# Kernel tuning notes

Measured on AMD Instinct MI355X. Metric: run time of the kernel, lower is better.

The kernel has to match this reference:

```python
import jax, jax.numpy as jnp
import numpy as np

B, T, I, H = 512, 512, 128, 256
EPS = 1e-5


def setup_inputs() -> dict:
    key = jax.random.key(0)
    ks = jax.random.split(key, 8)
    s_ih = 1.0 / np.sqrt(H)
    padded_X = jax.random.normal(ks[0], (B, T, I), dtype=jnp.float32)
    lengths = jax.random.randint(ks[1], (B,), 1, T + 1)  # in [1, T]
    # PyTorch LSTM params: W_ih (4H, I), W_hh (4H, H), biases (4H,), gate order [i,f,g,o]
    W_ih = jax.random.uniform(ks[2], (4 * H, I), minval=-s_ih, maxval=s_ih, dtype=jnp.float32)
    W_hh = jax.random.uniform(ks[3], (4 * H, H), minval=-s_ih, maxval=s_ih, dtype=jnp.float32)
    b_ih = jax.random.uniform(ks[4], (4 * H,), minval=-s_ih, maxval=s_ih, dtype=jnp.float32)
    b_hh = jax.random.uniform(ks[5], (4 * H,), minval=-s_ih, maxval=s_ih, dtype=jnp.float32)
    gamma = jnp.ones((H,), dtype=jnp.float32)
    beta = jnp.zeros((H,), dtype=jnp.float32)
    return {"padded_X": padded_X, "lengths": lengths, "W_ih": W_ih, "W_hh": W_hh,
            "b_ih": b_ih, "b_hh": b_hh, "gamma": gamma, "beta": beta}


def _lstm_last_hidden(padded_X, lengths, W_ih, W_hh, b_ih, b_hh):
    # Precompute input projections for all steps: (B, T, 4H)
    x_proj = jnp.einsum('bti,gi->btg', padded_X, W_ih) + b_ih + b_hh
    x_proj = jnp.swapaxes(x_proj, 0, 1)  # (T, B, 4H)
    ts = jnp.arange(padded_X.shape[1])

    def step(carry, inp):
        h, c = carry
        xp, t = inp
        gates = xp + h @ W_hh.T  # (B, 4H)
        i_g, f_g, g_g, o_g = jnp.split(gates, 4, axis=-1)
        i_g = jax.nn.sigmoid(i_g)
        f_g = jax.nn.sigmoid(f_g)
        g_g = jnp.tanh(g_g)
        o_g = jax.nn.sigmoid(o_g)
        c_new = f_g * c + i_g * g_g
        h_new = o_g * jnp.tanh(c_new)
        # freeze state once past the sequence length (packed-sequence semantics)
        valid = (t < lengths)[:, None]
        h = jnp.where(valid, h_new, h)
        c = jnp.where(valid, c_new, c)
        return (h, c), None

    h0 = jnp.zeros((padded_X.shape[0], W_hh.shape[1]), dtype=padded_X.dtype)
    c0 = jnp.zeros_like(h0)
    (h_fin, _), _ = jax.lax.scan(step, (h0, c0), (x_proj, ts))
    return h_fin  # (B, H) == h_n[-1]


def reference(padded_X, lengths, W_ih, W_hh, b_ih, b_hh, gamma, beta):
    h = _lstm_last_hidden(padded_X, lengths, W_ih, W_hh, b_ih, b_hh)
    mu = jnp.mean(h, axis=-1, keepdims=True)
    var = jnp.mean((h - mu) ** 2, axis=-1, keepdims=True)
    return (h - mu) / jnp.sqrt(var + EPS) * gamma + beta
```

## Files before the change

### kernel.cpp

```cpp
#include <hip/hip_runtime.h>

#define NB 512
#define NT 512
#define NI 128
#define NH 256
#define NG 1024
#define NMT 8
#define NWAVE 8
#define CH 8
#define EPSV 1e-5f

#define WXOFF 32768

typedef short short8 __attribute__((ext_vector_type(8)));
typedef float f32x4 __attribute__((ext_vector_type(4)));

__device__ __forceinline__ unsigned short f32_to_bf16(float f) {
  unsigned int u = __float_as_uint(f);
  u += 0x7fffu + ((u >> 16) & 1u);
  return (unsigned short)(u >> 16);
}
__device__ __forceinline__ float bf16_to_f32(unsigned short u) {
  return __uint_as_float(((unsigned int)u) << 16);
}

__global__ void prep_kernel(const float* __restrict__ W_ih, const float* __restrict__ W_hh,
                            const float* __restrict__ b_ih, const float* __restrict__ b_hh,
                            unsigned short* __restrict__ Wf, float* __restrict__ bsum) {
  int o = blockIdx.x * blockDim.x + threadIdx.x;
  int e = o & 7;
  int l = (o >> 3) & 63;
  int f = o >> 9;
  if (f < 512) {
    int kt = f & 7, m = (f >> 3) & 7, w = f >> 6;
    int row = w * 128 + m * 16 + (l & 15);
    int k = kt * 32 + ((l >> 4) << 3) + e;
    Wf[o] = f32_to_bf16(W_hh[row * NH + k]);
  } else if (f < 768) {
    int g = f - 512;
    int kx = g & 3, m = (g >> 2) & 7, w = g >> 5;
    int row = w * 128 + m * 16 + (l & 15);
    int k = kx * 32 + ((l >> 4) << 3) + e;
    Wf[o] = f32_to_bf16(W_ih[row * NI + k]);
  }
  if (o < NG) bsum[o] = b_ih[o] + b_hh[o];
}

__global__ void sort_kernel(const int* __restrict__ lengths, int* __restrict__ perm) {
  int i = threadIdx.x;
  __shared__ int L[NB];
  int li = lengths[i];
  L[i] = li;
  __syncthreads();
  int r = 0;
  for (int k = 0; k < NB; ++k) {
    int lk = L[k];
    r += (lk > li) || (lk == li && k < i);
  }
  perm[r] = i;
}

__global__ __launch_bounds__(512, 1)
void lstm_ln_kernel(const float* __restrict__ X, const int* __restrict__ lengths,
                    const int* __restrict__ perm,
                    const short8* __restrict__ Wf8, const float* __restrict__ bsum,
                    const float* __restrict__ gamma, const float* __restrict__ beta,
                    float* __restrict__ out) {
  const int p = blockIdx.x;
  const int tid = threadIdx.x;
  const int w = tid >> 6;
  const int l = tid & 63;

  __shared__ short8 ldsW[NWAVE * 14 * 64];
  __shared__ __align__(16) unsigned short gx[2 * CH][NG];
  __shared__ __align__(16) float gh[2][NG];
  __shared__ __align__(16) unsigned short hbuf[2][NH];
  __shared__ float red[20];

  const int b0 = perm[2 * p];
  const int b1 = perm[2 * p + 1];
  const int len0 = lengths[b0];
  const int len1 = lengths[b1];
  const int lmax = (len0 > len1) ? len0 : len1;

  short8 wreg[NMT][5];
#pragma unroll
  for (int m = 0; m < NMT; ++m)
#pragma unroll
    for (int kt = 0; kt < 5; ++kt)
      wreg[m][kt] = Wf8[((w * 8 + m) * 8 + kt) * 64 + l];
  short8 w6a = Wf8[((w * 8 + 6) * 8 + 6) * 64 + l];
  short8 w6b = Wf8[((w * 8 + 7) * 8 + 6) * 64 + l];
#pragma unroll
  for (int m = 0; m < NMT; ++m)
    ldsW[(w * 14 + m) * 64 + l] = Wf8[((w * 8 + m) * 8 + 5) * 64 + l];
#pragma unroll
  for (int m = 0; m < 6; ++m)
    ldsW[(w * 14 + 8 + m) * 64 + l] = Wf8[((w * 8 + m) * 8 + 6) * 64 + l];

  const int s = tid >> 8;
  const int j = tid & 255;
  const int mylen = s ? len1 : len0;
  const float bsi = bsum[j], bsf = bsum[NH + j], bsg = bsum[2 * NH + j], bso = bsum[3 * NH + j];
  float c = 0.f, h = 0.f;

  const float* __restrict__ xr0 = X + (size_t)b0 * NT * NI;
  const float* __restrict__ xr1 = X + (size_t)b1 * NT * NI;
  const int seqb = l & 1;
  const int kg = l >> 4;
  const int st = (l >> 1) & 7;
  const float* __restrict__ xp = seqb ? xr1 : xr0;

  hbuf[s][j] = 0;
  __syncthreads();

  for (int t = 0; t < lmax; ++t) {
    if ((t & 7) == 0) {
      const float* xb = xp + (size_t)(t + st) * NI + kg * 8;
      const int cc = l & 15;
#pragma unroll
      for (int half = 0; half < 2; ++half) {
        f32x4 ax[4];
#pragma unroll
        for (int m = 0; m < 4; ++m) ax[m] = (f32x4){0.f, 0.f, 0.f, 0.f};
#pragma unroll
        for (int kx = 0; kx < 4; ++kx) {
          float4 xa = *(const float4*)(xb + kx * 32);
          float4 xc = *(const float4*)(xb + kx * 32 + 4);
          short8 bx;
          bx[0] = (short)f32_to_bf16(xa.x); bx[1] = (short)f32_to_bf16(xa.y);
          bx[2] = (short)f32_to_bf16(xa.z); bx[3] = (short)f32_to_bf16(xa.w);
          bx[4] = (short)f32_to_bf16(xc.x); bx[5] = (short)f32_to_bf16(xc.y);
          bx[6] = (short)f32_to_bf16(xc.z); bx[7] = (short)f32_to_bf16(xc.w);
#pragma unroll
          for (int m = 0; m < 4; ++m) {
            short8 wi = Wf8[WXOFF + ((w * 8 + half * 4 + m) * 4 + kx) * 64 + l];
            ax[m] = __builtin_amdgcn_mfma_f32_16x16x32_bf16(wi, bx, ax[m], 0, 0, 0);
          }
        }
#pragma unroll
        for (int m = 0; m < 4; ++m) {
          int r0 = w * 128 + (half * 4 + m) * 16 + kg * 4;
          ushort4 pk;
          pk.x = f32_to_bf16(ax[m][0]); pk.y = f32_to_bf16(ax[m][1]);
          pk.z = f32_to_bf16(ax[m][2]); pk.w = f32_to_bf16(ax[m][3]);
          *(ushort4*)&gx[cc][r0] = pk;
        }
      }
    }

    f32x4 acc[NMT];
#pragma unroll
    for (int m = 0; m < NMT; ++m) acc[m] = (f32x4){0.f, 0.f, 0.f, 0.f};

#pragma unroll
    for (int kt = 0; kt < 5; ++kt) {
      short8 bh = *(const short8*)&hbuf[seqb][kt * 32 + kg * 8];
#pragma unroll
      for (int m = 0; m < NMT; ++m)
        acc[m] = __builtin_amdgcn_mfma_f32_16x16x32_bf16(wreg[m][kt], bh, acc[m], 0, 0, 0);
    }
    short8 sw[NMT];
#pragma unroll
    for (int m = 0; m < 4; ++m)
      sw[m] = Wf8[((w * 8 + m) * 8 + 7) * 64 + l];
    {
      short8 bh = *(const short8*)&hbuf[seqb][5 * 32 + kg * 8];
#pragma unroll
      for (int m = 0; m < NMT; ++m)
        acc[m] = __builtin_amdgcn_mfma_f32_16x16x32_bf16(ldsW[(w * 14 + m) * 64 + l], bh,
                                                         acc[m], 0, 0, 0);
    }
    short8 bh7 = *(const short8*)&hbuf[seqb][7 * 32 + kg * 8];
#pragma unroll
    for (int m = 0; m < 4; ++m)
      acc[m] = __builtin_amdgcn_mfma_f32_16x16x32_bf16(sw[m], bh7, acc[m], 0, 0, 0);
#pragma unroll
    for (int m = 4; m < 8; ++m)
      sw[m] = Wf8[((w * 8 + m) * 8 + 7) * 64 + l];
    {
      short8 bh = *(const short8*)&hbuf[seqb][6 * 32 + kg * 8];
#pragma unroll
      for (int m = 0; m < 6; ++m)
        acc[m] = __builtin_amdgcn_mfma_f32_16x16x32_bf16(ldsW[(w * 14 + 8 + m) * 64 + l], bh,
                                                         acc[m], 0, 0, 0);
      acc[6] = __builtin_amdgcn_mfma_f32_16x16x32_bf16(w6a, bh, acc[6], 0, 0, 0);
      acc[7] = __builtin_amdgcn_mfma_f32_16x16x32_bf16(w6b, bh, acc[7], 0, 0, 0);
    }
#pragma unroll
    for (int m = 4; m < 8; ++m)
      acc[m] = __builtin_amdgcn_mfma_f32_16x16x32_bf16(sw[m], bh7, acc[m], 0, 0, 0);

    if ((l & 15) < 2) {
#pragma unroll
      for (int m = 0; m < NMT; ++m)
        *(f32x4*)&gh[l & 1][w * 128 + m * 16 + kg * 4] = acc[m];
    }
    __syncthreads();

    {
      const int dt = ((t & 7) << 1) + s;
      float pi = gh[s][j]          + bf16_to_f32(gx[dt][j])          + bsi;
      float pf = gh[s][NH + j]     + bf16_to_f32(gx[dt][NH + j])     + bsf;
      float pg = gh[s][2 * NH + j] + bf16_to_f32(gx[dt][2 * NH + j]) + bsg;
      float po = gh[s][3 * NH + j] + bf16_to_f32(gx[dt][3 * NH + j]) + bso;
      if (t < mylen) {
        float ig = 1.f / (1.f + __expf(-pi));
        float fg = 1.f / (1.f + __expf(-pf));
        float gv = 1.f - 2.f / (1.f + __expf(2.f * pg));
        float og = 1.f / (1.f + __expf(-po));
        c = fg * c + ig * gv;
        h = og * (1.f - 2.f / (1.f + __expf(2.f * c)));
        hbuf[s][j] = f32_to_bf16(h);
      }
    }
    __syncthreads();
  }

  float sum = h, sq = h * h;
#pragma unroll
  for (int off = 32; off > 0; off >>= 1) {
    sum += __shfl_xor(sum, off);
    sq  += __shfl_xor(sq, off);
  }
  if (l == 0) { red[w] = sum; red[8 + w] = sq; }
  __syncthreads();
  if (tid == 0) {
    float S = red[0] + red[1] + red[2] + red[3];
    float Q = red[8] + red[9] + red[10] + red[11];
    float mu = S * (1.f / NH);
    red[16] = mu;
    red[17] = rsqrtf(Q * (1.f / NH) - mu * mu + EPSV);
  }
  if (tid == 256) {
    float S = red[4] + red[5] + red[6] + red[7];
    float Q = red[12] + red[13] + red[14] + red[15];
    float mu = S * (1.f / NH);
    red[18] = mu;
    red[19] = rsqrtf(Q * (1.f / NH) - mu * mu + EPSV);
  }
  __syncthreads();
  {
    float mu = red[16 + 2 * s], rstd = red[17 + 2 * s];
    int b = s ? b1 : b0;
    out[(size_t)b * NH + j] = (h - mu) * rstd * gamma[j] + beta[j];
  }
}

extern "C" void kernel_launch(void* const* d_in, const int* in_sizes, int n_in,
                              void* d_out, int out_size, void* d_ws, size_t ws_size,
                              hipStream_t stream) {
  const float* X       = (const float*)d_in[0];
  const int*   lengths = (const int*)d_in[1];
  const float* W_ih    = (const float*)d_in[2];
  const float* W_hh    = (const float*)d_in[3];
  const float* b_ih    = (const float*)d_in[4];
  const float* b_hh    = (const float*)d_in[5];
  const float* gamma   = (const float*)d_in[6];
  const float* beta    = (const float*)d_in[7];
  float* out = (float*)d_out;

  unsigned short* Wf = (unsigned short*)d_ws;
  float* bsum = (float*)((char*)d_ws + (size_t)768 * 512 * sizeof(unsigned short));
  int* perm = (int*)((char*)bsum + NG * sizeof(float));

  int total = 768 * 512;
  prep_kernel<<<(total + 255) / 256, 256, 0, stream>>>(W_ih, W_hh, b_ih, b_hh, Wf, bsum);
  sort_kernel<<<1, NB, 0, stream>>>(lengths, perm);
  lstm_ln_kernel<<<NB / 2, 512, 0, stream>>>(X, lengths, perm, (const short8*)Wf, bsum,
                                             gamma, beta, out);
}
```

Before: 2.687 ms.

## Halve input-projection chunk and rebalance W_hh across registers, LDS and global

Shrinks the input-projection chunk from 8 to 4 steps, so the x-projection MFMA work runs twice as often on half the rows and only half the lanes write results. Fewer W_hh k-tiles are kept in registers (4 instead of 5), two full k-tiles go to padded LDS, and two are streamed from global memory each step and issued early so their latency hides behind register MFMAs. The combined bias is folded into the bf16 gx values instead of being added per step, removing four per-thread bias registers. Register pressure drops, but the step loop now does more global weight loads and more frequent projection bursts, and the bias now passes through bf16 rounding.

```diff
diff --git a/kernel.cpp b/kernel.cpp
--- a/kernel.cpp
+++ b/kernel.cpp
@@ -7,7 +7,7 @@
 #define NG 1024
 #define NMT 8
 #define NWAVE 8
-#define CH 8
+#define CH 4
 #define EPSV 1e-5f
 
 #define WXOFF 32768
@@ -71,8 +71,8 @@
   const int w = tid >> 6;
   const int l = tid & 63;
 
-  __shared__ short8 ldsW[NWAVE * 14 * 64];
-  __shared__ __align__(16) unsigned short gx[2 * CH][NG];
+  __shared__ short8 ldsW[NWAVE * 16 * 64];
+  __shared__ __align__(16) unsigned short gx[2 * CH][NG + 8];
   __shared__ __align__(16) float gh[2][NG];
   __shared__ __align__(16) unsigned short hbuf[2][NH];
   __shared__ float red[20];
@@ -83,39 +83,35 @@
   const int len1 = lengths[b1];
   const int lmax = (len0 > len1) ? len0 : len1;
 
-  short8 wreg[NMT][5];
+  short8 wreg[NMT][4];
 #pragma unroll
   for (int m = 0; m < NMT; ++m)
 #pragma unroll
-    for (int kt = 0; kt < 5; ++kt)
+    for (int kt = 0; kt < 4; ++kt)
       wreg[m][kt] = Wf8[((w * 8 + m) * 8 + kt) * 64 + l];
-  short8 w6a = Wf8[((w * 8 + 6) * 8 + 6) * 64 + l];
-  short8 w6b = Wf8[((w * 8 + 7) * 8 + 6) * 64 + l];
-#pragma unroll
-  for (int m = 0; m < NMT; ++m)
-    ldsW[(w * 14 + m) * 64 + l] = Wf8[((w * 8 + m) * 8 + 5) * 64 + l];
-#pragma unroll
-  for (int m = 0; m < 6; ++m)
-    ldsW[(w * 14 + 8 + m) * 64 + l] = Wf8[((w * 8 + m) * 8 + 6) * 64 + l];
+#pragma unroll
+  for (int m = 0; m < NMT; ++m) {
+    ldsW[(w * 16 + m) * 64 + l]     = Wf8[((w * 8 + m) * 8 + 4) * 64 + l];
+    ldsW[(w * 16 + 8 + m) * 64 + l] = Wf8[((w * 8 + m) * 8 + 5) * 64 + l];
+  }
 
   const int s = tid >> 8;
   const int j = tid & 255;
   const int mylen = s ? len1 : len0;
-  const float bsi = bsum[j], bsf = bsum[NH + j], bsg = bsum[2 * NH + j], bso = bsum[3 * NH + j];
   float c = 0.f, h = 0.f;
 
   const float* __restrict__ xr0 = X + (size_t)b0 * NT * NI;
   const float* __restrict__ xr1 = X + (size_t)b1 * NT * NI;
   const int seqb = l & 1;
   const int kg = l >> 4;
-  const int st = (l >> 1) & 7;
+  const int st = (l >> 1) & 3;
   const float* __restrict__ xp = seqb ? xr1 : xr0;
 
   hbuf[s][j] = 0;
   __syncthreads();
 
   for (int t = 0; t < lmax; ++t) {
-    if ((t & 7) == 0) {
+    if ((t & 3) == 0) {
       const float* xb = xp + (size_t)(t + st) * NI + kg * 8;
       const int cc = l & 15;
 #pragma unroll
@@ -138,13 +134,16 @@
             ax[m] = __builtin_amdgcn_mfma_f32_16x16x32_bf16(wi, bx, ax[m], 0, 0, 0);
           }
         }
-#pragma unroll
-        for (int m = 0; m < 4; ++m) {
-          int r0 = w * 128 + (half * 4 + m) * 16 + kg * 4;
-          ushort4 pk;
-          pk.x = f32_to_bf16(ax[m][0]); pk.y = f32_to_bf16(ax[m][1]);
-          pk.z = f32_to_bf16(ax[m][2]); pk.w = f32_to_bf16(ax[m][3]);
-          *(ushort4*)&gx[cc][r0] = pk;
+        if (cc < 8) {
+#pragma unroll
+          for (int m = 0; m < 4; ++m) {
+            int r0 = w * 128 + (half * 4 + m) * 16 + kg * 4;
+            f32x4 bv = *(const f32x4*)&bsum[r0];
+            ushort4 pk;
+            pk.x = f32_to_bf16(ax[m][0] + bv[0]); pk.y = f32_to_bf16(ax[m][1] + bv[1]);
+            pk.z = f32_to_bf16(ax[m][2] + bv[2]); pk.w = f32_to_bf16(ax[m][3] + bv[3]);
+            *(ushort4*)&gx[cc][r0] = pk;
+          }
         }
       }
     }
@@ -153,43 +152,52 @@
 #pragma unroll
     for (int m = 0; m < NMT; ++m) acc[m] = (f32x4){0.f, 0.f, 0.f, 0.f};
 
-#pragma unroll
-    for (int kt = 0; kt < 5; ++kt) {
+    short8 swA[NMT];
+#pragma unroll
+    for (int m = 0; m < NMT; ++m) swA[m] = Wf8[((w * 8 + m) * 8 + 6) * 64 + l];
+
+#pragma unroll
+    for (int kt = 0; kt < 3; ++kt) {
       short8 bh = *(const short8*)&hbuf[seqb][kt * 32 + kg * 8];
 #pragma unroll
       for (int m = 0; m < NMT; ++m)
         acc[m] = __builtin_amdgcn_mfma_f32_16x16x32_bf16(wreg[m][kt], bh, acc[m], 0, 0, 0);
     }
-    short8 sw[NMT];
-#pragma unroll
-    for (int m = 0; m < 4; ++m)
-      sw[m] = Wf8[((w * 8 + m) * 8 + 7) * 64 + l];
+    {
+      short8 bh = *(const short8*)&hbuf[seqb][6 * 32 + kg * 8];
+#pragma unroll
+      for (int m = 0; m < NMT; ++m)
+        acc[m] = __builtin_amdgcn_mfma_f32_16x16x32_bf16(swA[m], bh, acc[m], 0, 0, 0);
+    }
+    short8 swB[NMT];
+#pragma unroll
+    for (int m = 0; m < NMT; ++m) swB[m] = Wf8[((w * 8 + m) * 8 + 7) * 64 + l];
+    {
+      short8 bh = *(const short8*)&hbuf[seqb][3 * 32 + kg * 8];
+#pragma unroll
+      for (int m = 0; m < NMT; ++m)
+        acc[m] = __builtin_amdgcn_mfma_f32_16x16x32_bf16(wreg[m][3], bh, acc[m], 0, 0, 0);
+    }
+    {
+      short8 bh = *(const short8*)&hbuf[seqb][4 * 32 + kg * 8];
+#pragma unroll
+      for (int m = 0; m < NMT; ++m)
+        acc[m] = __builtin_amdgcn_mfma_f32_16x16x32_bf16(ldsW[(w * 16 + m) * 64 + l], bh,
+                                                         acc[m], 0, 0, 0);
+    }
     {
       short8 bh = *(const short8*)&hbuf[seqb][5 * 32 + kg * 8];
 #pragma unroll
       for (int m = 0; m < NMT; ++m)
-        acc[m] = __builtin_amdgcn_mfma_f32_16x16x32_bf16(ldsW[(w * 14 + m) * 64 + l], bh,
+        acc[m] = __builtin_amdgcn_mfma_f32_16x16x32_bf16(ldsW[(w * 16 + 8 + m) * 64 + l], bh,
                                                          acc[m], 0, 0, 0);
     }
-    short8 bh7 = *(const short8*)&hbuf[seqb][7 * 32 + kg * 8];
-#pragma unroll
-    for (int m = 0; m < 4; ++m)
-      acc[m] = __builtin_amdgcn_mfma_f32_16x16x32_bf16(sw[m], bh7, acc[m], 0, 0, 0);
-#pragma unroll
-    for (int m = 4; m < 8; ++m)
-      sw[m] = Wf8[((w * 8 + m) * 8 + 7) * 64 + l];
-    {
-      short8 bh = *(const short8*)&hbuf[seqb][6 * 32 + kg * 8];
-#pragma unroll
-      for (int m = 0; m < 6; ++m)
-        acc[m] = __builtin_amdgcn_mfma_f32_16x16x32_bf16(ldsW[(w * 14 + 8 + m) * 64 + l], bh,
-                                                         acc[m], 0, 0, 0);
-      acc[6] = __builtin_amdgcn_mfma_f32_16x16x32_bf16(w6a, bh, acc[6], 0, 0, 0);
-      acc[7] = __builtin_amdgcn_mfma_f32_16x16x32_bf16(w6b, bh, acc[7], 0, 0, 0);
-    }
-#pragma unroll
-    for (int m = 4; m < 8; ++m)
-      acc[m] = __builtin_amdgcn_mfma_f32_16x16x32_bf16(sw[m], bh7, acc[m], 0, 0, 0);
+    {
+      short8 bh = *(const short8*)&hbuf[seqb][7 * 32 + kg * 8];
+#pragma unroll
+      for (int m = 0; m < NMT; ++m)
+        acc[m] = __builtin_amdgcn_mfma_f32_16x16x32_bf16(swB[m], bh, acc[m], 0, 0, 0);
+    }
 
     if ((l & 15) < 2) {
 #pragma unroll
@@ -199,11 +207,11 @@
     __syncthreads();
 
     {
-      const int dt = ((t & 7) << 1) + s;
-      float pi = gh[s][j]          + bf16_to_f32(gx[dt][j])          + bsi;
-      float pf = gh[s][NH + j]     + bf16_to_f32(gx[dt][NH + j])     + bsf;
-      float pg = gh[s][2 * NH + j] + bf16_to_f32(gx[dt][2 * NH + j]) + bsg;
-      float po = gh[s][3 * NH + j] + bf16_to_f32(gx[dt][3 * NH + j]) + bso;
+      const int dt = ((t & 3) << 1) + s;
+      float pi = gh[s][j]          + bf16_to_f32(gx[dt][j]);
+      float pf = gh[s][NH + j]     + bf16_to_f32(gx[dt][NH + j]);
+      float pg = gh[s][2 * NH + j] + bf16_to_f32(gx[dt][2 * NH + j]);
+      float po = gh[s][3 * NH + j] + bf16_to_f32(gx[dt][3 * NH + j]);
       if (t < mylen) {
         float ig = 1.f / (1.f + __expf(-pi));
         float fg = 1.f / (1.f + __expf(-pf));
```

Result: no change. 2.685 ms (-0.1%).
